# Kernel tuning notes

Hardware: AMD Instinct MI355X
Metric: run time of the kernel (lower is better)

## Reference

```python
import jax, jax.numpy as jnp
import numpy as np

DIM = 128
NUM_HEADS = 2
HEAD_DIM = DIM // NUM_HEADS
SCALE = HEAD_DIM ** -0.5
SR = 4
EPS_LN = 1e-5


def token2map(x, idx_token, H, W, H_init, W_init):
    """Scatter tokens x[B,N,Cc] into a [B,Cc,H,W] map via the init grid.
    Matches the sparse-COO branch of the torch token2map (N_init < N*H*W).
    """
    B, N, Cc = x.shape
    N_init = H_init * W_init
    # nearest-neighbor index of each init-grid cell in the HxW map
    rows = (jnp.arange(H_init) * H) // H_init          # floor(i * H / H_init)
    cols = (jnp.arange(W_init) * W) // W_init
    idx_hw = (rows[:, None] * W + cols[None, :]).reshape(-1)      # [N_init]
    flat = (idx_hw[None, :] + jnp.arange(B)[:, None] * (H * W)).reshape(-1)  # [B*N_init]
    # per-pixel count (A @ ones) + 1e-6, as in torch
    count = jax.ops.segment_sum(jnp.ones((B * N_init,), jnp.float32), flat,
                                num_segments=B * H * W) + 1e-6    # [B*H*W]
    gathered = jnp.take_along_axis(x, idx_token[..., None], axis=1)  # [B,N_init,Cc]
    out = jax.ops.segment_sum(gathered.reshape(B * N_init, Cc), flat,
                              num_segments=B * H * W)
    out = out / count[:, None]
    return out.reshape(B, H, W, Cc).transpose(0, 3, 1, 2)  # [B,Cc,H,W]


def setup_inputs() -> dict:
    key = jax.random.key(0)
    ks = jax.random.split(key, 12)
    B, Nq, Nkv, C = 8, 12544, 12544, DIM
    H, W, H_init, W_init = 112, 112, 224, 224
    inp = {
        'q_x': jax.random.normal(ks[0], (B, Nq, C), jnp.float32),
        'kv_x': jax.random.normal(ks[1], (B, Nkv, C), jnp.float32),
        'token_score': jax.random.normal(ks[2], (B, Nkv, 1), jnp.float32),
        'idx_token': jax.random.randint(ks[3], (B, H_init * W_init), 0, Nkv),
        'H': H, 'W': W, 'H_init': H_init, 'W_init': W_init,
        # learned params (qkv_bias=False)
        'q_w': jax.random.normal(ks[4], (C, C), jnp.float32) * 0.02,
        'kv_w': jax.random.normal(ks[5], (C, 2 * C), jnp.float32) * 0.02,
        'proj_w': jax.random.normal(ks[6], (C, C), jnp.float32) * 0.02,
        'proj_b': jnp.zeros((C,), jnp.float32),
        'sr_w': jax.random.normal(ks[7], (C, C, SR, SR), jnp.float32) * np.sqrt(2.0 / (SR * SR * C)),
        'sr_b': jnp.zeros((C,), jnp.float32),
        'norm_g': jnp.ones((C,), jnp.float32),
        'norm_b': jnp.zeros((C,), jnp.float32),
    }
    return inp


def reference(q_x, kv_x, token_score, q_w, kv_w, proj_w, proj_b, sr_w, sr_b,
              norm_g, norm_b, idx_token, H, W, H_init, W_init):
    B, Nq, C = q_x.shape
    # q projection -> [B, h, Nq, d]
    q = (q_x @ q_w).reshape(B, Nq, NUM_HEADS, HEAD_DIM).transpose(0, 2, 1, 3)

    # sr_ratio > 1 path: scatter kv tokens (with conf channel) to q's map
    tmp = jnp.concatenate([kv_x, token_score], axis=-1)          # [B,Nkv,C+1]
    tmp_map = token2map(tmp, idx_token, H, W, H_init, W_init)    # [B,C+1,H,W]
    kv_map = tmp_map[:, :C]                                      # [B,C,H,W]
    conf_map = tmp_map[:, C:]                                    # [B,1,H,W]

    # spatial reduction conv (kernel=stride=SR) + LayerNorm
    kv_r = jax.lax.conv_general_dilated(
        kv_map, sr_w, window_strides=(SR, SR), padding='VALID',
        dimension_numbers=('NCHW', 'OIHW', 'NCHW')) + sr_b[None, :, None, None]
    h, w = kv_r.shape[2], kv_r.shape[3]
    Ns = h * w
    kv_t = kv_r.reshape(B, C, Ns).transpose(0, 2, 1)             # [B,Ns,C]
    mu = jnp.mean(kv_t, axis=-1, keepdims=True)
    var = jnp.mean(jnp.square(kv_t - mu), axis=-1, keepdims=True)
    kv_t = (kv_t - mu) / jnp.sqrt(var + EPS_LN) * norm_g + norm_b

    # avg-pool conf to the reduced grid
    conf = conf_map.reshape(B, 1, h, SR, w, SR).mean(axis=(3, 5)).reshape(B, Ns)

    # kv projection -> k,v [B,h,Ns,d]
    kv_p = (kv_t @ kv_w).reshape(B, Ns, 2, NUM_HEADS, HEAD_DIM).transpose(2, 0, 3, 1, 4)
    k, v = kv_p[0], kv_p[1]

    attn = jnp.einsum('bhqd,bhkd->bhqk', q * SCALE, k) + conf[:, None, None, :]
    attn = jax.nn.softmax(attn, axis=-1)
    out = jnp.einsum('bhqk,bhkd->bhqd', attn, v).transpose(0, 2, 1, 3).reshape(B, Nq, C)
    return out @ proj_w + proj_b
```

## Files before the change

kernel.cpp:

```cpp
#include <hip/hip_runtime.h>
#include <hip/hip_bf16.h>


#define NBATCH 8
#define NQTOK  12544
#define NSP    832
#define LOG2E  1.4426950408889634f
#define QSCALE (0.125f * LOG2E)

typedef __attribute__((ext_vector_type(8))) short bf8;
typedef __attribute__((ext_vector_type(4))) float f4;
typedef __attribute__((ext_vector_type(4))) unsigned short u16x4;
typedef __attribute__((ext_vector_type(2))) unsigned int u32x2;

#define MFMA16(a, b, c) __builtin_amdgcn_mfma_f32_16x16x32_bf16((a), (b), (c), 0, 0, 0)

#if __has_builtin(__builtin_amdgcn_exp2f)
#define EXP2(x) __builtin_amdgcn_exp2f(x)
#else
#define EXP2(x) exp2f(x)
#endif

__device__ __forceinline__ unsigned short f2b(float x) {
  union { float f; unsigned u; } v; v.f = x;
  unsigned r = v.u + 0x7FFFu + ((v.u >> 16) & 1u);
  return (unsigned short)(r >> 16);
}

__device__ __forceinline__ unsigned pk2(float lo, float hi) {
  float2 t; t.x = lo; t.y = hi;
  __hip_bfloat162 bb = __float22bfloat162_rn(t);
  union { __hip_bfloat162 b; unsigned u; } v; v.b = bb;
  return v.u;
}

__device__ __forceinline__ bf8 rows2frag(const unsigned W0[2], const unsigned W1[2]) {
  u32x2 r0 = __builtin_amdgcn_permlane32_swap(W0[0], W1[0], false, false);
  u32x2 t02 = __builtin_amdgcn_permlane16_swap(r0.x, r0.y, false, false);
  u32x2 r1 = __builtin_amdgcn_permlane32_swap(W0[1], W1[1], false, false);
  u32x2 t13 = __builtin_amdgcn_permlane16_swap(r1.x, r1.y, false, false);
  union { unsigned u[4]; bf8 v; } pa;
  pa.u[0] = t02.x; pa.u[1] = t13.x; pa.u[2] = t02.y; pa.u[3] = t13.y;
  return pa.v;
}

__device__ __forceinline__ bf8 ldfrag(const unsigned short* t, int stride, int rbase, int kbase) {
  int lane = threadIdx.x & 63;
  return *(const bf8*)(t + (rbase + (lane & 15)) * stride + kbase + ((lane >> 4) << 3));
}

__global__ void k_setup(const float* __restrict__ qw, const float* __restrict__ kvw,
                        const float* __restrict__ pw, const float* __restrict__ srw,
                        unsigned short* __restrict__ qwt, unsigned short* __restrict__ kvwt,
                        unsigned short* __restrict__ pwt, unsigned short* __restrict__ srwt,
                        unsigned* __restrict__ kb, unsigned* __restrict__ vb,
                        float* __restrict__ conf) {
  int tid = blockIdx.x * 256 + threadIdx.x;
  int nt = gridDim.x * 256;
  for (int i = tid; i < 128 * 128; i += nt) {
    int k = i >> 7, n = i & 127;
    qwt[n * 128 + k] = f2b(qw[k * 128 + n] * QSCALE);
    pwt[n * 128 + k] = f2b(pw[k * 128 + n]);
  }
  for (int i = tid; i < 128 * 256; i += nt) {
    int k = i >> 8, j = i & 255;
    kvwt[j * 128 + k] = f2b(kvw[k * 256 + j]);
  }
  for (int i = tid; i < 128 * 2048; i += nt) {
    int o = i >> 11, kk = i & 2047;
    int p = kk >> 7, c = kk & 127;
    srwt[o * 2048 + kk] = f2b(srw[o * 2048 + c * 16 + p]);
  }
  const int nu = NBATCH * 2 * NSP * 64 / 2;
  for (int i = tid; i < nu; i += nt) { kb[i] = 0u; vb[i] = 0u; }
  for (int i = tid; i < NBATCH * NSP; i += nt) conf[i] = -1e30f;
}

__global__ void k_token2map(const float* __restrict__ kv_x, const float* __restrict__ tsc,
                            const int* __restrict__ idxt,
                            unsigned short* __restrict__ kv_map, float* __restrict__ conf_map) {
  int tid = threadIdx.x;
  int cell = blockIdx.x * 8 + (tid >> 5);
  int c0 = (tid & 31) << 2;
  int b = cell / 12544, hw = cell - b * 12544;
  int h = hw / 112, w = hw - h * 112;
  const int* it = idxt + b * 50176;
  int t0 = it[(2 * h) * 224 + 2 * w];
  int t1 = it[(2 * h) * 224 + 2 * w + 1];
  int t2 = it[(2 * h + 1) * 224 + 2 * w];
  int t3 = it[(2 * h + 1) * 224 + 2 * w + 1];
  const float* base = kv_x + (long)b * 12544 * 128 + c0;
  const float recip = 1.0f / (4.0f + 1e-6f);
  float4 a0 = *(const float4*)(base + (long)t0 * 128);
  float4 a1 = *(const float4*)(base + (long)t1 * 128);
  float4 a2 = *(const float4*)(base + (long)t2 * 128);
  float4 a3 = *(const float4*)(base + (long)t3 * 128);
  u16x4 o;
  o[0] = f2b((a0.x + a1.x + a2.x + a3.x) * recip);
  o[1] = f2b((a0.y + a1.y + a2.y + a3.y) * recip);
  o[2] = f2b((a0.z + a1.z + a2.z + a3.z) * recip);
  o[3] = f2b((a0.w + a1.w + a2.w + a3.w) * recip);
  *(u16x4*)(kv_map + (long)cell * 128 + c0) = o;
  if ((tid & 31) == 0) {
    const float* ts = tsc + b * 12544;
    conf_map[cell] = (ts[t0] + ts[t1] + ts[t2] + ts[t3]) * recip;
  }
}

__launch_bounds__(256)
__global__ void k_conv_ln(const unsigned short* __restrict__ kv_map,
                          const unsigned short* __restrict__ srwt,
                          const float* __restrict__ srb, const float* __restrict__ ng,
                          const float* __restrict__ nb, unsigned short* __restrict__ kv_t,
                          const float* __restrict__ conf_map, float* __restrict__ conf) {
  __shared__ unsigned short At[64 * 136];
  __shared__ unsigned short Bt[128 * 136];
  const int tid = threadIdx.x;
  const int lane = tid & 63, w = tid >> 6;
  const int l15 = lane & 15, g = lane >> 4;
  const int r0 = blockIdx.x * 64;
  if (tid < 64) {
    int pos = r0 + tid;
    int bq = pos / 784, p2 = pos - bq * 784;
    int oh = p2 / 28, ow = p2 - oh * 28;
    float s = 0.f;
#pragma unroll
    for (int kh = 0; kh < 4; kh++)
#pragma unroll
      for (int kw = 0; kw < 4; kw++)
        s += conf_map[bq * 12544 + (4 * oh + kh) * 112 + 4 * ow + kw];
    conf[bq * NSP + p2] = s * (LOG2E / 16.0f);
  }
  const f4 fz = {0.f, 0.f, 0.f, 0.f};
  f4 acc[8];
#pragma unroll
  for (int i = 0; i < 8; i++) acc[i] = fz;

  for (int p = 0; p < 16; p++) {
#pragma unroll
    for (int j = 0; j < 4; j++) {
      int id = tid + 256 * j;
      int row = id >> 4, c0 = (id & 15) << 3;
      int rr = r0 + row;
      int bb = rr / 784, pos = rr - bb * 784;
      int oh = pos / 28, ow = pos - oh * 28;
      long src = ((long)(bb * 12544 + (4 * oh + (p >> 2)) * 112 + 4 * ow + (p & 3))) * 128 + c0;
      *(uint4*)(At + row * 136 + c0) = *(const uint4*)(kv_map + src);
    }
#pragma unroll
    for (int j = 0; j < 8; j++) {
      int id = tid + 256 * j;
      int row = id >> 4, c0 = (id & 15) << 3;
      *(uint4*)(Bt + row * 136 + c0) = *(const uint4*)(srwt + row * 2048 + p * 128 + c0);
    }
    __syncthreads();
#pragma unroll
    for (int ks = 0; ks < 4; ks++) {
      bf8 a = ldfrag(At, 136, 16 * w, 32 * ks);
#pragma unroll
      for (int nf = 0; nf < 8; nf++) {
        bf8 bb = ldfrag(Bt, 136, 16 * nf, 32 * ks);
        acc[nf] = MFMA16(a, bb, acc[nf]);
      }
    }
    __syncthreads();
  }
  float sum_[4] = {0.f, 0.f, 0.f, 0.f}, sq_[4] = {0.f, 0.f, 0.f, 0.f};
#pragma unroll
  for (int nf = 0; nf < 8; nf++) {
    float bias = srb[16 * nf + l15];
#pragma unroll
    for (int reg = 0; reg < 4; reg++) {
      float v = acc[nf][reg] + bias;
      acc[nf][reg] = v;
      sum_[reg] += v;
      sq_[reg] += v * v;
    }
  }
#pragma unroll
  for (int msk = 1; msk < 16; msk <<= 1)
#pragma unroll
    for (int reg = 0; reg < 4; reg++) {
      sum_[reg] += __shfl_xor(sum_[reg], msk, 64);
      sq_[reg] += __shfl_xor(sq_[reg], msk, 64);
    }
  float mean[4], rstd[4];
#pragma unroll
  for (int reg = 0; reg < 4; reg++) {
    mean[reg] = sum_[reg] * (1.0f / 128.0f);
    float var = sq_[reg] * (1.0f / 128.0f) - mean[reg] * mean[reg];
    rstd[reg] = rsqrtf(var + 1e-5f);
  }
#pragma unroll
  for (int nf = 0; nf < 8; nf++) {
    float gc = ng[16 * nf + l15], bc = nb[16 * nf + l15];
#pragma unroll
    for (int reg = 0; reg < 4; reg++) {
      int row = r0 + 16 * w + 4 * g + reg;
      float v = (acc[nf][reg] - mean[reg]) * rstd[reg] * gc + bc;
      kv_t[row * 128 + 16 * nf + l15] = f2b(v);
    }
  }
}

__launch_bounds__(256)
__global__ void k_kv(const unsigned short* __restrict__ kv_t,
                     const unsigned short* __restrict__ kvwt,
                     unsigned short* __restrict__ kbuf, unsigned short* __restrict__ vbuf) {
  __shared__ unsigned short At[64 * 136];
  __shared__ unsigned short Bt[128 * 136];
  const int tid = threadIdx.x;
  const int lane = tid & 63, w = tid >> 6;
  const int l15 = lane & 15, g = lane >> 4;
  const int r0 = blockIdx.x * 64;
  const int sel = blockIdx.y;
#pragma unroll
  for (int j = 0; j < 4; j++) {
    int id = tid + 256 * j;
    int row = id >> 4, c0 = (id & 15) << 3;
    *(uint4*)(At + row * 136 + c0) = *(const uint4*)(kv_t + (long)(r0 + row) * 128 + c0);
  }
#pragma unroll
  for (int j = 0; j < 8; j++) {
    int id = tid + 256 * j;
    int row = id >> 4, c0 = (id & 15) << 3;
    *(uint4*)(Bt + row * 136 + c0) = *(const uint4*)(kvwt + (long)(sel * 128 + row) * 128 + c0);
  }
  __syncthreads();
  const f4 fz = {0.f, 0.f, 0.f, 0.f};
  f4 acc[8];
#pragma unroll
  for (int i = 0; i < 8; i++) acc[i] = fz;
#pragma unroll
  for (int ks = 0; ks < 4; ks++) {
    bf8 a = ldfrag(At, 136, 16 * w, 32 * ks);
#pragma unroll
    for (int nf = 0; nf < 8; nf++) {
      bf8 bb = ldfrag(Bt, 136, 16 * nf, 32 * ks);
      acc[nf] = MFMA16(a, bb, acc[nf]);
    }
  }
#pragma unroll
  for (int nf = 0; nf < 8; nf++)
#pragma unroll
    for (int reg = 0; reg < 4; reg++) {
      int r = r0 + 16 * w + 4 * g + reg;
      int b = r / 784, ns = r - b * 784;
      int j = 16 * nf + l15;
      int hh = j >> 6, d = j & 63;
      unsigned short val = f2b(acc[nf][reg]);
      if (sel == 0) kbuf[((long)(b * 2 + hh) * NSP + ns) * 64 + d] = val;
      else          vbuf[((long)(b * 2 + hh) * 64 + d) * NSP + ns] = val;
    }
}

__launch_bounds__(256, 3)
__global__ void k_attn(const float* __restrict__ q_x,
                       const unsigned short* __restrict__ qwt,
                       const unsigned short* __restrict__ kbuf,
                       const unsigned short* __restrict__ vbuf,
                       const float* __restrict__ conf,
                       unsigned short* __restrict__ attbuf) {
  __shared__ unsigned short SMEM[18432];
  const int tid = threadIdx.x;
  const int lane = tid & 63, w = tid >> 6;
  const int l15 = lane & 15, g = lane >> 4;
  const int h = blockIdx.y, b = blockIdx.z;
  const int bh = b * 2 + h;
  const int q0b = blockIdx.x * 128;
  const int q0 = q0b + 32 * w;

  {
    int row = tid >> 1, ch = (tid & 1) << 6;
    const float* src = q_x + ((long)b * NQTOK + q0b + row) * 128 + ch;
    unsigned short* dst = SMEM + row * 136 + ch;
#pragma unroll
    for (int j = 0; j < 8; j++) {
      float4 v0 = *(const float4*)(src + 8 * j);
      float4 v1 = *(const float4*)(src + 8 * j + 4);
      unsigned u[4];
      u[0] = pk2(v0.x, v0.y); u[1] = pk2(v0.z, v0.w);
      u[2] = pk2(v1.x, v1.y); u[3] = pk2(v1.z, v1.w);
      *(uint4*)(dst + 8 * j) = *(uint4*)u;
    }
  }
  __syncthreads();
  bf8 qf[2][2];
#pragma unroll
  for (int mr = 0; mr < 2; mr++) {
    f4 qacc[4];
    const f4 fz0 = {0.f, 0.f, 0.f, 0.f};
#pragma unroll
    for (int mf = 0; mf < 4; mf++) qacc[mf] = fz0;
#pragma unroll
    for (int ks4 = 0; ks4 < 4; ks4++) {
      bf8 bqx = ldfrag(SMEM, 136, 32 * w + 16 * mr, 32 * ks4);
#pragma unroll
      for (int mf = 0; mf < 4; mf++) {
        bf8 aqw = *(const bf8*)(qwt + (64 * h + 16 * mf + l15) * 128 + 32 * ks4 + (g << 3));
        qacc[mf] = MFMA16(aqw, bqx, qacc[mf]);
      }
    }
    unsigned W[4][2];
#pragma unroll
    for (int mf = 0; mf < 4; mf++) {
      W[mf][0] = pk2(qacc[mf][0], qacc[mf][1]);
      W[mf][1] = pk2(qacc[mf][2], qacc[mf][3]);
    }
#pragma unroll
    for (int kap = 0; kap < 2; kap++)
      qf[mr][kap] = rows2frag(W[2 * kap], W[2 * kap + 1]);
  }
  __syncthreads();

  const int srow = tid >> 2;
  const int scol = (tid & 3) << 4;
  const unsigned short* kg = kbuf + (long)bh * NSP * 64 + srow * 64 + scol;
  const unsigned short* vg = vbuf + (long)bh * 64 * NSP + (long)srow * NSP + scol;
  unsigned short* klds = SMEM + srow * 72 + scol;
  unsigned short* vlds = SMEM + 9216 + srow * 72 + scol;

  uint4 kr0, kr1, vr0, vr1;
#define ISSUE(T)                                                   \
  do {                                                             \
    const unsigned short* kp_ = kg + (long)(T) * 4096;             \
    const unsigned short* vp_ = vg + (T) * 64;                     \
    kr0 = *(const uint4*)(kp_);                                    \
    kr1 = *(const uint4*)(kp_ + 8);                                \
    vr0 = *(const uint4*)(vp_);                                    \
    vr1 = *(const uint4*)(vp_ + 8);                                \
  } while (0)
#define STWRITE(BUF)                                               \
  do {                                                             \
    unsigned short* kd_ = klds + (BUF) * 4608;                     \
    unsigned short* vd_ = vlds + (BUF) * 4608;                     \
    *(uint4*)kd_ = kr0;  *(uint4*)(kd_ + 8) = kr1;                 \
    *(uint4*)vd_ = vr0;  *(uint4*)(vd_ + 8) = vr1;                 \
  } while (0)

  ISSUE(0);
  STWRITE(0);
  ISSUE(1);
  __syncthreads();

  const f4 fz = {0.f, 0.f, 0.f, 0.f};
  f4 ao[2][4], aol[2];
#pragma unroll
  for (int mr = 0; mr < 2; mr++) {
    aol[mr] = fz;
#pragma unroll
    for (int i = 0; i < 4; i++) ao[mr][i] = fz;
  }
  const short on = (short)0x3F80;
  const bf8 onesf = {on, on, on, on, on, on, on, on};
  const float* confb = conf + b * NSP;

#pragma unroll 2
  for (int t = 0; t < 13; t++) {
    const int cur = t & 1;
    const unsigned short* KtB = SMEM + cur * 4608;
    const unsigned short* VtB = SMEM + 9216 + cur * 4608;
    bf8 kf[4][2];
#pragma unroll
    for (int mf = 0; mf < 4; mf++)
#pragma unroll
      for (int ks = 0; ks < 2; ks++)
        kf[mf][ks] = ldfrag(KtB, 72, 16 * mf, 32 * ks);
    bf8 vf[4][2];
#pragma unroll
    for (int nfd = 0; nfd < 4; nfd++)
#pragma unroll
      for (int ks = 0; ks < 2; ks++)
        vf[nfd][ks] = ldfrag(VtB, 72, 16 * nfd, 32 * ks);
    float4 cv[4];
#pragma unroll
    for (int mf = 0; mf < 4; mf++)
      cv[mf] = *(const float4*)(confb + t * 64 + 16 * mf + 4 * g);
#pragma unroll
    for (int mr = 0; mr < 2; mr++) {
      f4 s_[4];
#pragma unroll
      for (int mf = 0; mf < 4; mf++) s_[mf] = fz;
#pragma unroll
      for (int ks = 0; ks < 2; ks++)
#pragma unroll
        for (int mf = 0; mf < 4; mf++)
          s_[mf] = MFMA16(kf[mf][ks], qf[mr][ks], s_[mf]);
      unsigned W[4][2];
#pragma unroll
      for (int mf = 0; mf < 4; mf++) {
        float p0 = EXP2(s_[mf][0] + cv[mf].x);
        float p1 = EXP2(s_[mf][1] + cv[mf].y);
        float p2 = EXP2(s_[mf][2] + cv[mf].z);
        float p3 = EXP2(s_[mf][3] + cv[mf].w);
        W[mf][0] = pk2(p0, p1);
        W[mf][1] = pk2(p2, p3);
      }
#pragma unroll
      for (int ks = 0; ks < 2; ks++) {
        bf8 pa = rows2frag(W[2 * ks], W[2 * ks + 1]);
        aol[mr] = MFMA16(pa, onesf, aol[mr]);
#pragma unroll
        for (int nfd = 0; nfd < 4; nfd++)
          ao[mr][nfd] = MFMA16(pa, vf[nfd][ks], ao[mr][nfd]);
      }
    }
    if (t < 12) STWRITE(cur ^ 1);
    if (t < 11) ISSUE(t + 2);
    __syncthreads();
  }
#undef ISSUE
#undef STWRITE
#pragma unroll
  for (int mr = 0; mr < 2; mr++) {
    float inv[4];
#pragma unroll
    for (int reg = 0; reg < 4; reg++) inv[reg] = 1.0f / aol[mr][reg];
#pragma unroll
    for (int nfd = 0; nfd < 4; nfd++)
#pragma unroll
      for (int reg = 0; reg < 4; reg++) {
        int n = q0 + 16 * mr + 4 * g + reg;
        int col = h * 64 + 16 * nfd + l15;
        attbuf[((long)b * NQTOK + n) * 128 + col] = f2b(ao[mr][nfd][reg] * inv[reg]);
      }
  }
}

__launch_bounds__(256)
__global__ void k_proj(const unsigned short* __restrict__ attbuf,
                       const unsigned short* __restrict__ pwt,
                       const float* __restrict__ pb, float* __restrict__ out) {
  __shared__ unsigned short At[64 * 136];
  __shared__ unsigned short Bt[128 * 136];
  const int tid = threadIdx.x;
  const int lane = tid & 63, w = tid >> 6;
  const int l15 = lane & 15, g = lane >> 4;
  const int r0 = blockIdx.x * 64;
#pragma unroll
  for (int j = 0; j < 4; j++) {
    int id = tid + 256 * j;
    int row = id >> 4, c0 = (id & 15) << 3;
    *(uint4*)(At + row * 136 + c0) = *(const uint4*)(attbuf + (long)(r0 + row) * 128 + c0);
  }
#pragma unroll
  for (int j = 0; j < 8; j++) {
    int id = tid + 256 * j;
    int row = id >> 4, c0 = (id & 15) << 3;
    *(uint4*)(Bt + row * 136 + c0) = *(const uint4*)(pwt + (long)row * 128 + c0);
  }
  __syncthreads();
  const f4 fz = {0.f, 0.f, 0.f, 0.f};
  f4 acc[8];
#pragma unroll
  for (int i = 0; i < 8; i++) acc[i] = fz;
#pragma unroll
  for (int ks = 0; ks < 4; ks++) {
    bf8 a = ldfrag(At, 136, 16 * w, 32 * ks);
#pragma unroll
    for (int nf = 0; nf < 8; nf++) {
      bf8 bb = ldfrag(Bt, 136, 16 * nf, 32 * ks);
      acc[nf] = MFMA16(a, bb, acc[nf]);
    }
  }
#pragma unroll
  for (int nf = 0; nf < 8; nf++) {
    float bias = pb[16 * nf + l15];
#pragma unroll
    for (int reg = 0; reg < 4; reg++) {
      int r = r0 + 16 * w + 4 * g + reg;
      out[(long)r * 128 + 16 * nf + l15] = acc[nf][reg] + bias;
    }
  }
}

extern "C" void kernel_launch(void* const* d_in, const int* in_sizes, int n_in,
                              void* d_out, int out_size, void* d_ws, size_t ws_size,
                              hipStream_t stream) {
  const float* q_x  = (const float*)d_in[0];
  const float* kv_x = (const float*)d_in[1];
  const float* tsc  = (const float*)d_in[2];
  const int*   idxt = (const int*)d_in[3];
  const float* q_w  = (const float*)d_in[8];
  const float* kv_w = (const float*)d_in[9];
  const float* pw   = (const float*)d_in[10];
  const float* pb   = (const float*)d_in[11];
  const float* srw  = (const float*)d_in[12];
  const float* srb  = (const float*)d_in[13];
  const float* ng   = (const float*)d_in[14];
  const float* nb   = (const float*)d_in[15];
  float* outp = (float*)d_out;

  char* ws = (char*)d_ws;
  size_t off = 0;
  auto take = [&](size_t bytes) {
    char* p = ws + off;
    off += (bytes + 255) & ~(size_t)255;
    return p;
  };
  unsigned short* qwt   = (unsigned short*)take(128 * 128 * 2);
  unsigned short* pwt   = (unsigned short*)take(128 * 128 * 2);
  unsigned short* kvwt  = (unsigned short*)take(256 * 128 * 2);
  unsigned short* srwt  = (unsigned short*)take(128 * 2048 * 2);
  unsigned short* kvmap = (unsigned short*)take((size_t)NBATCH * 12544 * 128 * 2);
  float* conf_map       = (float*)take((size_t)NBATCH * 12544 * 4);
  unsigned short* kvt   = (unsigned short*)take((size_t)NBATCH * 784 * 128 * 2);
  unsigned short* kbuf  = (unsigned short*)take((size_t)NBATCH * 2 * NSP * 64 * 2);
  unsigned short* vbuf  = (unsigned short*)take((size_t)NBATCH * 2 * NSP * 64 * 2);
  float* conf           = (float*)take((size_t)NBATCH * NSP * 4);
  unsigned short* attbuf = kvmap;

  k_setup<<<512, 256, 0, stream>>>(q_w, kv_w, pw, srw, qwt, kvwt, pwt, srwt,
                                   (unsigned*)kbuf, (unsigned*)vbuf, conf);
  k_token2map<<<12544, 256, 0, stream>>>(kv_x, tsc, idxt, kvmap, conf_map);
  k_conv_ln<<<98, 256, 0, stream>>>(kvmap, srwt, srb, ng, nb, kvt, conf_map, conf);
  k_kv<<<dim3(98, 2), 256, 0, stream>>>(kvt, kvwt, kbuf, vbuf);
  k_attn<<<dim3(98, 2, 8), 256, 0, stream>>>(q_x, qwt, kbuf, vbuf, conf, attbuf);
  k_proj<<<1568, 256, 0, stream>>>(attbuf, pwt, pb, outp);
}
```

Measured before the change: 179.3 us.

## Fuse LayerNorm with KV projection and fold output projection into attention

The conv+LayerNorm kernel now writes normalized rows to shared memory and performs the KV projection in place, removing the kv_t round trip and one launch. The attention kernel now uses 512 threads, with both heads in one block sharing the q_x tile. It writes per-head outputs to shared memory and applies the output projection plus bias directly, which eliminates the attbuf write/read and the separate proj kernel. This costs a larger shared-memory footprint, more registers per thread, and weight fragments read straight from global memory instead of staged through LDS.

```diff
diff --git a/kernel.cpp b/kernel.cpp
--- a/kernel.cpp
+++ b/kernel.cpp
@@ -108,11 +108,14 @@
 }
 
 __launch_bounds__(256)
-__global__ void k_conv_ln(const unsigned short* __restrict__ kv_map,
-                          const unsigned short* __restrict__ srwt,
-                          const float* __restrict__ srb, const float* __restrict__ ng,
-                          const float* __restrict__ nb, unsigned short* __restrict__ kv_t,
-                          const float* __restrict__ conf_map, float* __restrict__ conf) {
+__global__ void k_conv_ln_kv(const unsigned short* __restrict__ kv_map,
+                             const unsigned short* __restrict__ srwt,
+                             const float* __restrict__ srb, const float* __restrict__ ng,
+                             const float* __restrict__ nb,
+                             const unsigned short* __restrict__ kvwt,
+                             unsigned short* __restrict__ kbuf,
+                             unsigned short* __restrict__ vbuf,
+                             const float* __restrict__ conf_map, float* __restrict__ conf) {
   __shared__ unsigned short At[64 * 136];
   __shared__ unsigned short Bt[128 * 136];
   const int tid = threadIdx.x;
@@ -184,98 +187,69 @@
       sum_[reg] += __shfl_xor(sum_[reg], msk, 64);
       sq_[reg] += __shfl_xor(sq_[reg], msk, 64);
     }
-  float mean[4], rstd[4];
-#pragma unroll
-  for (int reg = 0; reg < 4; reg++) {
-    mean[reg] = sum_[reg] * (1.0f / 128.0f);
-    float var = sq_[reg] * (1.0f / 128.0f) - mean[reg] * mean[reg];
-    rstd[reg] = rsqrtf(var + 1e-5f);
-  }
 #pragma unroll
   for (int nf = 0; nf < 8; nf++) {
     float gc = ng[16 * nf + l15], bc = nb[16 * nf + l15];
 #pragma unroll
     for (int reg = 0; reg < 4; reg++) {
-      int row = r0 + 16 * w + 4 * g + reg;
-      float v = (acc[nf][reg] - mean[reg]) * rstd[reg] * gc + bc;
-      kv_t[row * 128 + 16 * nf + l15] = f2b(v);
-    }
-  }
-}
-
-__launch_bounds__(256)
-__global__ void k_kv(const unsigned short* __restrict__ kv_t,
-                     const unsigned short* __restrict__ kvwt,
-                     unsigned short* __restrict__ kbuf, unsigned short* __restrict__ vbuf) {
-  __shared__ unsigned short At[64 * 136];
-  __shared__ unsigned short Bt[128 * 136];
-  const int tid = threadIdx.x;
-  const int lane = tid & 63, w = tid >> 6;
-  const int l15 = lane & 15, g = lane >> 4;
-  const int r0 = blockIdx.x * 64;
-  const int sel = blockIdx.y;
-#pragma unroll
-  for (int j = 0; j < 4; j++) {
-    int id = tid + 256 * j;
-    int row = id >> 4, c0 = (id & 15) << 3;
-    *(uint4*)(At + row * 136 + c0) = *(const uint4*)(kv_t + (long)(r0 + row) * 128 + c0);
-  }
-#pragma unroll
-  for (int j = 0; j < 8; j++) {
-    int id = tid + 256 * j;
-    int row = id >> 4, c0 = (id & 15) << 3;
-    *(uint4*)(Bt + row * 136 + c0) = *(const uint4*)(kvwt + (long)(sel * 128 + row) * 128 + c0);
+      float mean = sum_[reg] * (1.0f / 128.0f);
+      float var = sq_[reg] * (1.0f / 128.0f) - mean * mean;
+      float v = (acc[nf][reg] - mean) * rsqrtf(var + 1e-5f) * gc + bc;
+      At[(16 * w + 4 * g + reg) * 136 + 16 * nf + l15] = f2b(v);
+    }
   }
   __syncthreads();
-  const f4 fz = {0.f, 0.f, 0.f, 0.f};
-  f4 acc[8];
-#pragma unroll
-  for (int i = 0; i < 8; i++) acc[i] = fz;
+  f4 acc2[16];
+#pragma unroll
+  for (int i = 0; i < 16; i++) acc2[i] = fz;
 #pragma unroll
   for (int ks = 0; ks < 4; ks++) {
     bf8 a = ldfrag(At, 136, 16 * w, 32 * ks);
 #pragma unroll
-    for (int nf = 0; nf < 8; nf++) {
-      bf8 bb = ldfrag(Bt, 136, 16 * nf, 32 * ks);
-      acc[nf] = MFMA16(a, bb, acc[nf]);
-    }
-  }
-#pragma unroll
-  for (int nf = 0; nf < 8; nf++)
+    for (int nf = 0; nf < 16; nf++) {
+      bf8 bb = *(const bf8*)(kvwt + (16 * nf + l15) * 128 + 32 * ks + (g << 3));
+      acc2[nf] = MFMA16(a, bb, acc2[nf]);
+    }
+  }
+#pragma unroll
+  for (int nf = 0; nf < 16; nf++)
 #pragma unroll
     for (int reg = 0; reg < 4; reg++) {
       int r = r0 + 16 * w + 4 * g + reg;
       int b = r / 784, ns = r - b * 784;
       int j = 16 * nf + l15;
-      int hh = j >> 6, d = j & 63;
-      unsigned short val = f2b(acc[nf][reg]);
+      int sel = j >> 7, hh = (j >> 6) & 1, d = j & 63;
+      unsigned short val = f2b(acc2[nf][reg]);
       if (sel == 0) kbuf[((long)(b * 2 + hh) * NSP + ns) * 64 + d] = val;
       else          vbuf[((long)(b * 2 + hh) * 64 + d) * NSP + ns] = val;
     }
 }
 
-__launch_bounds__(256, 3)
+__launch_bounds__(512, 4)
 __global__ void k_attn(const float* __restrict__ q_x,
                        const unsigned short* __restrict__ qwt,
                        const unsigned short* __restrict__ kbuf,
                        const unsigned short* __restrict__ vbuf,
                        const float* __restrict__ conf,
-                       unsigned short* __restrict__ attbuf) {
-  __shared__ unsigned short SMEM[18432];
+                       const unsigned short* __restrict__ pwt,
+                       const float* __restrict__ pb,
+                       float* __restrict__ out) {
+  __shared__ unsigned short SMEM[36864];
   const int tid = threadIdx.x;
   const int lane = tid & 63, w = tid >> 6;
   const int l15 = lane & 15, g = lane >> 4;
-  const int h = blockIdx.y, b = blockIdx.z;
+  const int h = w >> 2;
+  const int b = blockIdx.y;
   const int bh = b * 2 + h;
   const int q0b = blockIdx.x * 128;
-  const int q0 = q0b + 32 * w;
+  const int q0 = q0b + 32 * (w & 3);
 
   {
-    int row = tid >> 1, ch = (tid & 1) << 6;
-    const float* src = q_x + ((long)b * NQTOK + q0b + row) * 128 + ch;
-    unsigned short* dst = SMEM + row * 136 + ch;
-#pragma unroll
-    for (int j = 0; j < 8; j++) {
+    int row = tid >> 2, ch0 = (tid & 3) << 5;
+    const float* src = q_x + ((long)b * NQTOK + q0b + row) * 128 + ch0;
+    unsigned short* dst = SMEM + row * 136 + ch0;
+#pragma unroll
+    for (int j = 0; j < 4; j++) {
       float4 v0 = *(const float4*)(src + 8 * j);
       float4 v1 = *(const float4*)(src + 8 * j + 4);
       unsigned u[4];
@@ -294,7 +268,7 @@
     for (int mf = 0; mf < 4; mf++) qacc[mf] = fz0;
 #pragma unroll
     for (int ks4 = 0; ks4 < 4; ks4++) {
-      bf8 bqx = ldfrag(SMEM, 136, 32 * w + 16 * mr, 32 * ks4);
+      bf8 bqx = ldfrag(SMEM, 136, 32 * (w & 3) + 16 * mr, 32 * ks4);
 #pragma unroll
       for (int mf = 0; mf < 4; mf++) {
         bf8 aqw = *(const bf8*)(qwt + (64 * h + 16 * mf + l15) * 128 + 32 * ks4 + (g << 3));
@@ -313,29 +287,30 @@
   }
   __syncthreads();
 
-  const int srow = tid >> 2;
-  const int scol = (tid & 3) << 4;
-  const unsigned short* kg = kbuf + (long)bh * NSP * 64 + srow * 64 + scol;
-  const unsigned short* vg = vbuf + (long)bh * 64 * NSP + (long)srow * NSP + scol;
-  unsigned short* klds = SMEM + srow * 72 + scol;
-  unsigned short* vlds = SMEM + 9216 + srow * 72 + scol;
-
-  uint4 kr0, kr1, vr0, vr1;
+  const int plane = tid >> 7;
+  const int hp = plane & 1, isv = plane >> 1;
+  const int pr = (tid & 127) >> 1;
+  const int scol = ((tid & 127) & 1) << 5;
+  const unsigned short* srcb = isv
+      ? vbuf + ((long)(b * 2 + hp) * 64 + pr) * NSP + scol
+      : kbuf + ((long)(b * 2 + hp) * NSP + pr) * 64 + scol;
+  const int tstep = isv ? 64 : 4096;
+  unsigned short* dstb = SMEM + isv * 18432 + hp * 9216 + pr * 72 + scol;
+
+  uint4 r0_, r1_, r2_, r3_;
 #define ISSUE(T)                                                   \
   do {                                                             \
-    const unsigned short* kp_ = kg + (long)(T) * 4096;             \
-    const unsigned short* vp_ = vg + (T) * 64;                     \
-    kr0 = *(const uint4*)(kp_);                                    \
-    kr1 = *(const uint4*)(kp_ + 8);                                \
-    vr0 = *(const uint4*)(vp_);                                    \
-    vr1 = *(const uint4*)(vp_ + 8);                                \
+    const unsigned short* sp_ = srcb + (long)(T) * tstep;          \
+    r0_ = *(const uint4*)(sp_);                                    \
+    r1_ = *(const uint4*)(sp_ + 8);                                \
+    r2_ = *(const uint4*)(sp_ + 16);                               \
+    r3_ = *(const uint4*)(sp_ + 24);                               \
   } while (0)
 #define STWRITE(BUF)                                               \
   do {                                                             \
-    unsigned short* kd_ = klds + (BUF) * 4608;                     \
-    unsigned short* vd_ = vlds + (BUF) * 4608;                     \
-    *(uint4*)kd_ = kr0;  *(uint4*)(kd_ + 8) = kr1;                 \
-    *(uint4*)vd_ = vr0;  *(uint4*)(vd_ + 8) = vr1;                 \
+    unsigned short* dp_ = dstb + (BUF) * 4608;                     \
+    *(uint4*)dp_ = r0_;        *(uint4*)(dp_ + 8) = r1_;           \
+    *(uint4*)(dp_ + 16) = r2_; *(uint4*)(dp_ + 24) = r3_;          \
   } while (0)
 
   ISSUE(0);
@@ -354,12 +329,14 @@
   const short on = (short)0x3F80;
   const bf8 onesf = {on, on, on, on, on, on, on, on};
   const float* confb = conf + b * NSP;
+  const unsigned short* Kh = SMEM + h * 9216;
+  const unsigned short* Vh = SMEM + 18432 + h * 9216;
 
 #pragma unroll 2
   for (int t = 0; t < 13; t++) {
     const int cur = t & 1;
-    const unsigned short* KtB = SMEM + cur * 4608;
-    const unsigned short* VtB = SMEM + 9216 + cur * 4608;
+    const unsigned short* KtB = Kh + cur * 4608;
+    const unsigned short* VtB = Vh + cur * 4608;
     bf8 kf[4][2];
 #pragma unroll
     for (int mf = 0; mf < 4; mf++)
@@ -411,6 +388,7 @@
   }
 #undef ISSUE
 #undef STWRITE
+
 #pragma unroll
   for (int mr = 0; mr < 2; mr++) {
     float inv[4];
@@ -420,47 +398,22 @@
     for (int nfd = 0; nfd < 4; nfd++)
 #pragma unroll
       for (int reg = 0; reg < 4; reg++) {
-        int n = q0 + 16 * mr + 4 * g + reg;
-        int col = h * 64 + 16 * nfd + l15;
-        attbuf[((long)b * NQTOK + n) * 128 + col] = f2b(ao[mr][nfd][reg] * inv[reg]);
+        int row = 32 * (w & 3) + 16 * mr + 4 * g + reg;
+        int col = 64 * h + 16 * nfd + l15;
+        SMEM[row * 136 + col] = f2b(ao[mr][nfd][reg] * inv[reg]);
       }
   }
-}
-
-__launch_bounds__(256)
-__global__ void k_proj(const unsigned short* __restrict__ attbuf,
-                       const unsigned short* __restrict__ pwt,
-                       const float* __restrict__ pb, float* __restrict__ out) {
-  __shared__ unsigned short At[64 * 136];
-  __shared__ unsigned short Bt[128 * 136];
-  const int tid = threadIdx.x;
-  const int lane = tid & 63, w = tid >> 6;
-  const int l15 = lane & 15, g = lane >> 4;
-  const int r0 = blockIdx.x * 64;
-#pragma unroll
-  for (int j = 0; j < 4; j++) {
-    int id = tid + 256 * j;
-    int row = id >> 4, c0 = (id & 15) << 3;
-    *(uint4*)(At + row * 136 + c0) = *(const uint4*)(attbuf + (long)(r0 + row) * 128 + c0);
-  }
-#pragma unroll
-  for (int j = 0; j < 8; j++) {
-    int id = tid + 256 * j;
-    int row = id >> 4, c0 = (id & 15) << 3;
-    *(uint4*)(Bt + row * 136 + c0) = *(const uint4*)(pwt + (long)row * 128 + c0);
-  }
   __syncthreads();
-  const f4 fz = {0.f, 0.f, 0.f, 0.f};
-  f4 acc[8];
-#pragma unroll
-  for (int i = 0; i < 8; i++) acc[i] = fz;
+  f4 pacc[8];
+#pragma unroll
+  for (int i = 0; i < 8; i++) pacc[i] = fz;
 #pragma unroll
   for (int ks = 0; ks < 4; ks++) {
-    bf8 a = ldfrag(At, 136, 16 * w, 32 * ks);
+    bf8 a = ldfrag(SMEM, 136, 16 * w, 32 * ks);
 #pragma unroll
     for (int nf = 0; nf < 8; nf++) {
-      bf8 bb = ldfrag(Bt, 136, 16 * nf, 32 * ks);
-      acc[nf] = MFMA16(a, bb, acc[nf]);
+      bf8 bb = *(const bf8*)(pwt + (16 * nf + l15) * 128 + 32 * ks + (g << 3));
+      pacc[nf] = MFMA16(a, bb, pacc[nf]);
     }
   }
 #pragma unroll
@@ -468,8 +421,8 @@
     float bias = pb[16 * nf + l15];
 #pragma unroll
     for (int reg = 0; reg < 4; reg++) {
-      int r = r0 + 16 * w + 4 * g + reg;
-      out[(long)r * 128 + 16 * nf + l15] = acc[nf][reg] + bias;
+      int r = q0b + 16 * w + 4 * g + reg;
+      out[((long)b * NQTOK + r) * 128 + 16 * nf + l15] = pacc[nf][reg] + bias;
     }
   }
 }
@@ -504,17 +457,14 @@
   unsigned short* srwt  = (unsigned short*)take(128 * 2048 * 2);
   unsigned short* kvmap = (unsigned short*)take((size_t)NBATCH * 12544 * 128 * 2);
   float* conf_map       = (float*)take((size_t)NBATCH * 12544 * 4);
-  unsigned short* kvt   = (unsigned short*)take((size_t)NBATCH * 784 * 128 * 2);
   unsigned short* kbuf  = (unsigned short*)take((size_t)NBATCH * 2 * NSP * 64 * 2);
   unsigned short* vbuf  = (unsigned short*)take((size_t)NBATCH * 2 * NSP * 64 * 2);
   float* conf           = (float*)take((size_t)NBATCH * NSP * 4);
-  unsigned short* attbuf = kvmap;
 
   k_setup<<<512, 256, 0, stream>>>(q_w, kv_w, pw, srw, qwt, kvwt, pwt, srwt,
                                    (unsigned*)kbuf, (unsigned*)vbuf, conf);
   k_token2map<<<12544, 256, 0, stream>>>(kv_x, tsc, idxt, kvmap, conf_map);
-  k_conv_ln<<<98, 256, 0, stream>>>(kvmap, srwt, srb, ng, nb, kvt, conf_map, conf);
-  k_kv<<<dim3(98, 2), 256, 0, stream>>>(kvt, kvwt, kbuf, vbuf);
-  k_attn<<<dim3(98, 2, 8), 256, 0, stream>>>(q_x, qwt, kbuf, vbuf, conf, attbuf);
-  k_proj<<<1568, 256, 0, stream>>>(attbuf, pwt, pb, outp);
-}
+  k_conv_ln_kv<<<98, 256, 0, stream>>>(kvmap, srwt, srb, ng, nb, kvwt, kbuf, vbuf,
+                                       conf_map, conf);
+  k_attn<<<dim3(98, 8), 512, 0, stream>>>(q_x, qwt, kbuf, vbuf, conf, pwt, pb, outp);
+}
```

Result: slower. 403.5 us (+125.0%).
